# Kernel tuning notes

Hardware: AMD Instinct MI355X
Metric: run time of the kernel (lower is better)

The kernel has to match this reference:

```python
import jax, jax.numpy as jnp
import numpy as np

EPS = 1e-5

def _bn_relu(y, mean, var, scale, bias):
    # y: (b, c, n); eval-mode batchnorm over channel axis, then ReLU
    inv = scale / jnp.sqrt(var + EPS)
    return jax.nn.relu((y - mean[None, :, None]) * inv[None, :, None] + bias[None, :, None])

def setup_inputs() -> dict:
    key = jax.random.key(0)
    ks = jax.random.split(key, 6)
    b, c, n, cr = 4, 256, 4096, 32
    inp = {
        'x': jax.random.normal(ks[0], (b, c, n), jnp.float32),
        'w_q': jax.random.normal(ks[1], (cr, c), jnp.float32) * (1.0 / np.sqrt(c)),
        'w_k': jax.random.normal(ks[2], (cr, c), jnp.float32) * (1.0 / np.sqrt(c)),
        'w_v': jax.random.normal(ks[3], (c, c), jnp.float32) * (1.0 / np.sqrt(c)),
        'bn1_scale': jnp.ones((cr,), jnp.float32), 'bn1_bias': jnp.zeros((cr,), jnp.float32),
        'bn1_mean': jnp.zeros((cr,), jnp.float32), 'bn1_var': jnp.ones((cr,), jnp.float32),
        'bn2_scale': jnp.ones((cr,), jnp.float32), 'bn2_bias': jnp.zeros((cr,), jnp.float32),
        'bn2_mean': jnp.zeros((cr,), jnp.float32), 'bn2_var': jnp.ones((cr,), jnp.float32),
        'bn3_scale': jnp.ones((c,), jnp.float32), 'bn3_bias': jnp.zeros((c,), jnp.float32),
        'bn3_mean': jnp.zeros((c,), jnp.float32), 'bn3_var': jnp.ones((c,), jnp.float32),
        'gamma': jax.random.normal(ks[4], (1,), jnp.float32),
    }
    return inp

def reference(x, w_q, w_k, w_v,
              bn1_scale, bn1_bias, bn1_mean, bn1_var,
              bn2_scale, bn2_bias, bn2_mean, bn2_var,
              bn3_scale, bn3_bias, bn3_mean, bn3_var,
              gamma):
    # x: (b, c, n). Original views as (b, c, n, 1) so width=1, height=n.
    b, c, n = x.shape
    # 1x1 conv == channel matmul, then BN+ReLU
    q = _bn_relu(jnp.einsum('oc,bcn->bon', w_q, x), bn1_mean, bn1_var, bn1_scale, bn1_bias)  # (b, c', n)
    k = _bn_relu(jnp.einsum('oc,bcn->bon', w_k, x), bn2_mean, bn2_var, bn2_scale, bn2_bias)  # (b, c', n)
    v = _bn_relu(jnp.einsum('oc,bcn->bon', w_v, x), bn3_mean, bn3_var, bn3_scale, bn3_bias)  # (b, c, n)
    # energy_H: (b, n, n) with -inf diagonal (self-attention along 'height')
    energy_h = jnp.einsum('bdi,bdj->bij', q, k)
    eye = jnp.eye(n, dtype=bool)
    energy_h = jnp.where(eye[None], -jnp.inf, energy_h)
    # energy_W: width=1 -> per-position self energy (b, n)
    energy_w = jnp.sum(q * k, axis=1)
    # softmax over concat of n H-logits and 1 W-logit
    att = jax.nn.softmax(jnp.concatenate([energy_h, energy_w[..., None]], axis=-1), axis=-1)  # (b, n, n+1)
    att_h = att[..., :n]        # (b, n, n), query i -> key j
    att_w = att[..., n]         # (b, n)
    out_h = jnp.einsum('bcj,bij->bci', v, att_h)   # aggregate values along height
    out_w = v * att_w[:, None, :]                  # width=1 self term
    out = gamma[0] * (out_h + out_w) + x
    return out
```

## Files before the change

### kernel.cpp

```cpp
#include <hip/hip_runtime.h>
#include <math.h>

#define Bb 4
#define Cc 256
#define Nn 4096
#define CR 32
#define EPS_BN 1e-5f
#define SHIFT 20.0f
#define JSPLIT 4
#define JSL (Nn / JSPLIT)
#define TJ 64
#define NTILES (JSL / TJ)

typedef __attribute__((ext_vector_type(8))) short short8;
typedef __attribute__((ext_vector_type(4))) float f32x4;

__device__ inline unsigned int pk2(float a, float b) {
    __bf16 ha = (__bf16)a, hb = (__bf16)b;
    unsigned short ra = __builtin_bit_cast(unsigned short, ha);
    unsigned short rb = __builtin_bit_cast(unsigned short, hb);
    return ((unsigned int)rb << 16) | ra;
}
__device__ inline float blo(unsigned int u) { return __uint_as_float(u << 16); }
__device__ inline float bhi(unsigned int u) { return __uint_as_float(u & 0xffff0000u); }

__global__ __launch_bounds__(256) void xt_kernel(
    const float* __restrict__ x, __bf16* __restrict__ xTh, __bf16* __restrict__ xTl)
{
    __shared__ float sT[64][68];
    const int tid = threadIdx.x;
    const int n0 = blockIdx.x * 64, c0 = blockIdx.y * 64, b = blockIdx.z;
    const int n4 = tid & 15, cr = tid >> 4;
#pragma unroll
    for (int it = 0; it < 4; ++it) {
        int cl = cr + it * 16;
        float4 t = *(const float4*)&x[(size_t)(b * Cc + c0 + cl) * Nn + n0 + n4 * 4];
        *(float4*)&sT[cl][n4 * 4] = t;
    }
    __syncthreads();
    const int nl = tid >> 2, cq = tid & 3;
    float hv[16], lv[16];
#pragma unroll
    for (int e = 0; e < 16; ++e) {
        float v = sT[cq * 16 + e][nl];
        float h = (float)(__bf16)v;
        hv[e] = h; lv[e] = v - h;
    }
    uint4 H0 = { pk2(hv[0],hv[1]), pk2(hv[2],hv[3]), pk2(hv[4],hv[5]), pk2(hv[6],hv[7]) };
    uint4 H1 = { pk2(hv[8],hv[9]), pk2(hv[10],hv[11]), pk2(hv[12],hv[13]), pk2(hv[14],hv[15]) };
    uint4 L0 = { pk2(lv[0],lv[1]), pk2(lv[2],lv[3]), pk2(lv[4],lv[5]), pk2(lv[6],lv[7]) };
    uint4 L1 = { pk2(lv[8],lv[9]), pk2(lv[10],lv[11]), pk2(lv[12],lv[13]), pk2(lv[14],lv[15]) };
    size_t row = (size_t)(b * Nn + n0 + nl) * Cc + c0 + cq * 16;
    *(uint4*)&xTh[row] = H0; *(uint4*)&xTh[row + 8] = H1;
    *(uint4*)&xTl[row] = L0; *(uint4*)&xTl[row + 8] = L1;
}

__global__ __launch_bounds__(256) void qkv_kernel(
    const __bf16* __restrict__ xTh, const __bf16* __restrict__ xTl,
    const float* __restrict__ wq, const float* __restrict__ wk, const float* __restrict__ wv,
    const float* __restrict__ bn1s, const float* __restrict__ bn1b, const float* __restrict__ bn1m, const float* __restrict__ bn1v,
    const float* __restrict__ bn2s, const float* __restrict__ bn2b, const float* __restrict__ bn2m, const float* __restrict__ bn2v,
    const float* __restrict__ bn3s, const float* __restrict__ bn3b, const float* __restrict__ bn3m, const float* __restrict__ bn3v,
    __bf16* __restrict__ Qt, __bf16* __restrict__ Kt, __bf16* __restrict__ Vb)
{
    __shared__ __align__(16) __bf16 sW[64 * 264];

    const int tid = threadIdx.x;
    const int n0 = blockIdx.x * 128, g = blockIdx.y, b = blockIdx.z;
    const int lane = tid & 63, w = tid >> 6;
    const int l15 = lane & 15, l4 = lane >> 4;

    {
        int r = tid >> 2, q = tid & 3;
        int R = g * 64 + r;
        const float* src = (R < 32) ? (wq + (size_t)R * Cc)
                         : (R < 64) ? (wk + (size_t)(R - 32) * Cc)
                                    : (wv + (size_t)(R - 64) * Cc);
#pragma unroll
        for (int u8 = 0; u8 < 8; ++u8) {
            float4 a = *(const float4*)&src[q * 64 + u8 * 8];
            float4 c2 = *(const float4*)&src[q * 64 + u8 * 8 + 4];
            uint4 p = { pk2(a.x,a.y), pk2(a.z,a.w), pk2(c2.x,c2.y), pk2(c2.z,c2.w) };
            *(uint4*)&sW[r * 264 + q * 64 + u8 * 8] = p;
        }
    }
    __syncthreads();

    short8 af[8];
#pragma unroll
    for (int kc = 0; kc < 8; ++kc)
        af[kc] = *(const short8*)&sW[(w * 16 + l15) * 264 + kc * 32 + l4 * 8];

    f32x4 acc[8];
#pragma unroll
    for (int z = 0; z < 8; ++z) acc[z] = (f32x4){0.f, 0.f, 0.f, 0.f};

#pragma unroll
    for (int kc = 0; kc < 8; ++kc) {
#pragma unroll
        for (int nt = 0; nt < 8; ++nt) {
            size_t base = (size_t)(b * Nn + n0 + nt * 16 + l15) * Cc + kc * 32 + l4 * 8;
            short8 bh = *(const short8*)&xTh[base];
            short8 bl = *(const short8*)&xTl[base];
            acc[nt] = __builtin_amdgcn_mfma_f32_16x16x32_bf16(af[kc], bh, acc[nt], 0, 0, 0);
            acc[nt] = __builtin_amdgcn_mfma_f32_16x16x32_bf16(af[kc], bl, acc[nt], 0, 0, 0);
        }
    }

    float scl[4], off[4];
#pragma unroll
    for (int r = 0; r < 4; ++r) {
        int R = g * 64 + w * 16 + l4 * 4 + r;
        const float *bs, *bbi, *bm, *bv2; int row;
        if (R < 32)      { row = R;      bs = bn1s; bbi = bn1b; bm = bn1m; bv2 = bn1v; }
        else if (R < 64) { row = R - 32; bs = bn2s; bbi = bn2b; bm = bn2m; bv2 = bn2v; }
        else             { row = R - 64; bs = bn3s; bbi = bn3b; bm = bn3m; bv2 = bn3v; }
        float s = bs[row] / sqrtf(bv2[row] + EPS_BN);
        scl[r] = s; off[r] = bbi[row] - bm[row] * s;
    }

    if (g == 0) {
        __bf16* dst = (w < 2) ? Qt : Kt;
        int d0 = (w & 1) * 16 + l4 * 4;
#pragma unroll
        for (int nt = 0; nt < 8; ++nt) {
            f32x4 a = acc[nt];
            float e0 = fmaxf(fmaf(a.x, scl[0], off[0]), 0.f);
            float e1 = fmaxf(fmaf(a.y, scl[1], off[1]), 0.f);
            float e2 = fmaxf(fmaf(a.z, scl[2], off[2]), 0.f);
            float e3 = fmaxf(fmaf(a.w, scl[3], off[3]), 0.f);
            uint2 p = { pk2(e0, e1), pk2(e2, e3) };
            int n = n0 + nt * 16 + l15;
            *(uint2*)&dst[(size_t)(b * Nn + n) * CR + d0] = p;
        }
    } else {
        __bf16* oT = sW;
        __syncthreads();
#pragma unroll
        for (int nt = 0; nt < 8; ++nt) {
            f32x4 a = acc[nt];
            float e[4];
            e[0] = fmaxf(fmaf(a.x, scl[0], off[0]), 0.f);
            e[1] = fmaxf(fmaf(a.y, scl[1], off[1]), 0.f);
            e[2] = fmaxf(fmaf(a.z, scl[2], off[2]), 0.f);
            e[3] = fmaxf(fmaf(a.w, scl[3], off[3]), 0.f);
#pragma unroll
            for (int r = 0; r < 4; ++r)
                oT[(w * 16 + l4 * 4 + r) * 136 + nt * 16 + l15] = (__bf16)e[r];
        }
        __syncthreads();
        int rr = tid >> 2, qq = tid & 3;
        size_t vrow = (size_t)(b * Cc + (g - 1) * 64 + rr) * Nn + n0 + qq * 32;
#pragma unroll
        for (int e8 = 0; e8 < 4; ++e8)
            *(uint4*)&Vb[vrow + e8 * 8] = *(const uint4*)&oT[rr * 136 + qq * 32 + e8 * 8];
    }
}

__global__ __launch_bounds__(256) void attn_kernel(
    const __bf16* __restrict__ Qt, const __bf16* __restrict__ Kt,
    const __bf16* __restrict__ Vb,
    __bf16* __restrict__ PO, float* __restrict__ PL)
{
    __shared__ __align__(16) __bf16 sQ[64 * 40];
    __shared__ __align__(16) __bf16 sP[64 * 72];
    __shared__ __align__(16) float  sL[4][64];

    const int tid = threadIdx.x, lane = tid & 63, w = tid >> 6;
    const int b = blockIdx.z, js = blockIdx.y, i0 = blockIdx.x * 64;
    const int l15 = lane & 15, l4 = lane >> 4;

    {
        int i = tid >> 2, o = tid & 3;
        *(uint4*)&sQ[i * 40 + o * 8] =
            *(const uint4*)&Qt[(size_t)(b * Nn + i0 + i) * CR + o * 8];
    }
    __syncthreads();
    short8 qf[4];
#pragma unroll
    for (int it = 0; it < 4; ++it)
        qf[it] = *(const short8*)&sQ[(it * 16 + l15) * 40 + l4 * 8];

    f32x4 oacc[16];
#pragma unroll
    for (int z = 0; z < 16; ++z) oacc[z] = (f32x4){0.f, 0.f, 0.f, 0.f};
    float lp[4] = {0.f, 0.f, 0.f, 0.f};

    const size_t jb = (size_t)js * JSL;
    short8 kf = *(const short8*)&Kt[(size_t)(b * Nn + jb + 16 * w + l15) * CR + l4 * 8];

    for (int t = 0; t < NTILES; ++t) {
        const size_t j0 = jb + (size_t)t * TJ;

        short8 vf[8];
#pragma unroll
        for (int u = 0; u < 8; ++u) {
            int jh = u >> 2, ct = u & 3;
            int c = w * 64 + ct * 16 + l15;
            vf[u] = *(const short8*)&Vb[(size_t)(b * Cc + c) * Nn + j0 + (jh * 4 + l4) * 8];
        }

#pragma unroll
        for (int it = 0; it < 4; ++it) {
            f32x4 c0 = (f32x4){0.f, 0.f, 0.f, 0.f};
            c0 = __builtin_amdgcn_mfma_f32_16x16x32_bf16(kf, qf[it], c0, 0, 0, 0);
            float e0 = __expf(c0.x - SHIFT);
            float e1 = __expf(c0.y - SHIFT);
            float e2 = __expf(c0.z - SHIFT);
            float e3 = __expf(c0.w - SHIFT);
            lp[it] += (e0 + e1) + (e2 + e3);
            uint2 p2 = { pk2(e0, e1), pk2(e2, e3) };
            *(uint2*)&sP[(it * 16 + l15) * 72 + w * 16 + l4 * 4] = p2;
        }
        __syncthreads();

        if (t + 1 < NTILES)
            kf = *(const short8*)&Kt[(size_t)(b * Nn + j0 + TJ + 16 * w + l15) * CR + l4 * 8];

#pragma unroll
        for (int jh = 0; jh < 2; ++jh) {
            short8 pf[4];
#pragma unroll
            for (int it = 0; it < 4; ++it)
                pf[it] = *(const short8*)&sP[(it * 16 + l15) * 72 + jh * 32 + l4 * 8];
#pragma unroll
            for (int ct = 0; ct < 4; ++ct) {
#pragma unroll
                for (int it = 0; it < 4; ++it)
                    oacc[it * 4 + ct] = __builtin_amdgcn_mfma_f32_16x16x32_bf16(
                        pf[it], vf[jh * 4 + ct], oacc[it * 4 + ct], 0, 0, 0);
            }
        }
        __syncthreads();
    }

#pragma unroll
    for (int it = 0; it < 4; ++it) {
        float v = lp[it];
        v += __shfl_xor(v, 16);
        v += __shfl_xor(v, 32);
        if (lane < 16) sL[w][it * 16 + lane] = v;
    }
    __syncthreads();
    if (tid < 64)
        PL[(size_t)(js * Bb + b) * Nn + i0 + tid] =
            sL[0][tid] + sL[1][tid] + sL[2][tid] + sL[3][tid];

    const size_t base = (size_t)((js * Bb + b) * (Nn / 64) + blockIdx.x) * 16384;
#pragma unroll
    for (int it = 0; it < 4; ++it)
#pragma unroll
        for (int ct = 0; ct < 4; ++ct) {
            f32x4 a = oacc[it * 4 + ct];
            uint2 p = { pk2(a.x, a.y), pk2(a.z, a.w) };
            *(uint2*)&PO[base + (size_t)((((w * 4 + it) * 4 + ct) * 64 + lane)) * 4] = p;
        }
}

__global__ __launch_bounds__(256) void reduce_kernel(
    const __bf16* __restrict__ PO, const float* __restrict__ PL,
    const float* __restrict__ x, const float* __restrict__ gamma,
    float* __restrict__ out)
{
    __shared__ __align__(16) float oT[64 * 68];
    __shared__ float sLinv[64];

    const int tid = threadIdx.x;
    const int iblk = blockIdx.x, wq = blockIdx.y, b = blockIdx.z;
    const int i0 = iblk * 64;
    const int lane = tid & 63, ct = tid >> 6, l15 = lane & 15, l4 = lane >> 4;

    if (tid < 64) {
        float l = 0.f;
#pragma unroll
        for (int js = 0; js < JSPLIT; ++js)
            l += PL[(size_t)(js * Bb + b) * Nn + i0 + tid];
        sLinv[tid] = 1.0f / l;
    }

    float o[4][4];
#pragma unroll
    for (int it = 0; it < 4; ++it) {
        o[it][0] = o[it][1] = o[it][2] = o[it][3] = 0.f;
#pragma unroll
        for (int js = 0; js < JSPLIT; ++js) {
            size_t base = (size_t)((js * Bb + b) * (Nn / 64) + iblk) * 16384;
            uint2 v = *(const uint2*)&PO[base + (size_t)((((wq * 4 + it) * 4 + ct) * 64 + lane)) * 4];
            o[it][0] += blo(v.x); o[it][1] += bhi(v.x);
            o[it][2] += blo(v.y); o[it][3] += bhi(v.y);
        }
    }

    const int cl = ct * 16 + l15;
#pragma unroll
    for (int it = 0; it < 4; ++it) {
        float4 t4 = { o[it][0], o[it][1], o[it][2], o[it][3] };
        *(float4*)&oT[cl * 68 + it * 16 + l4 * 4] = t4;
    }
    __syncthreads();

    const float g = gamma[0];
    const int c_l = tid >> 2, icol = (tid & 3) * 16;
    const int cg = wq * 64 + c_l;
    const size_t gb = (size_t)(b * Cc + cg) * Nn + i0 + icol;
#pragma unroll
    for (int k4 = 0; k4 < 4; ++k4) {
        float4 ov = *(const float4*)&oT[c_l * 68 + icol + k4 * 4];
        float4 li = *(const float4*)&sLinv[icol + k4 * 4];
        float4 xv = *(const float4*)&x[gb + k4 * 4];
        float4 res;
        res.x = fmaf(g, ov.x * li.x, xv.x);
        res.y = fmaf(g, ov.y * li.y, xv.y);
        res.z = fmaf(g, ov.z * li.z, xv.z);
        res.w = fmaf(g, ov.w * li.w, xv.w);
        *(float4*)&out[gb + k4 * 4] = res;
    }
}

extern "C" void kernel_launch(void* const* d_in, const int* in_sizes, int n_in,
                              void* d_out, int out_size, void* d_ws, size_t ws_size,
                              hipStream_t stream)
{
    const float* x    = (const float*)d_in[0];
    const float* wq   = (const float*)d_in[1];
    const float* wk   = (const float*)d_in[2];
    const float* wv   = (const float*)d_in[3];
    const float* bn1s = (const float*)d_in[4];
    const float* bn1b = (const float*)d_in[5];
    const float* bn1m = (const float*)d_in[6];
    const float* bn1v = (const float*)d_in[7];
    const float* bn2s = (const float*)d_in[8];
    const float* bn2b = (const float*)d_in[9];
    const float* bn2m = (const float*)d_in[10];
    const float* bn2v = (const float*)d_in[11];
    const float* bn3s = (const float*)d_in[12];
    const float* bn3b = (const float*)d_in[13];
    const float* bn3m = (const float*)d_in[14];
    const float* bn3v = (const float*)d_in[15];
    const float* gmm  = (const float*)d_in[16];
    float* out = (float*)d_out;

    char* ws = (char*)d_ws;
    __bf16* Qt  = (__bf16*)(ws);
    __bf16* Kt  = (__bf16*)(ws + (1u << 20));
    __bf16* Vb  = (__bf16*)(ws + (2u << 20));
    char*   big = ws + (10u << 20);
    __bf16* xTh = (__bf16*)big;
    __bf16* xTl = (__bf16*)(big + 8388608);
    __bf16* PO  = (__bf16*)big;
    float*  PL  = (float*)(big + 33554432);

    xt_kernel<<<dim3(Nn / 64, Cc / 64, Bb), 256, 0, stream>>>(x, xTh, xTl);

    qkv_kernel<<<dim3(Nn / 128, 5, Bb), 256, 0, stream>>>(
        xTh, xTl, wq, wk, wv,
        bn1s, bn1b, bn1m, bn1v,
        bn2s, bn2b, bn2m, bn2v,
        bn3s, bn3b, bn3m, bn3v,
        Qt, Kt, Vb);

    attn_kernel<<<dim3(Nn / 64, JSPLIT, Bb), 256, 0, stream>>>(Qt, Kt, Vb, PO, PL);

    reduce_kernel<<<dim3(Nn / 64, 4, Bb), 256, 0, stream>>>(PO, PL, x, gmm, out);
}
```

Baseline: 235.9 us.

## Remap attention blocks per XCD, stage x tiles in LDS, use exp2 softmax

The attention grid is flattened and remapped so that blocks sharing a (j-split, batch) pair land on the same XCD, which should improve L2 reuse of K and V. The QKV kernel now stages x hi/lo tiles through shared memory with register prefetch instead of reading them directly from global memory, at the cost of two barriers per k-chunk. K is prescaled by log2(e) so the softmax can use native exp2 with an adjusted shift. The transpose kernel rotates its LDS read order to reduce bank conflicts, and the BN scale uses rsqrt instead of a division.

```diff
diff --git a/kernel.cpp b/kernel.cpp
--- a/kernel.cpp
+++ b/kernel.cpp
@@ -1,12 +1,12 @@
 #include <hip/hip_runtime.h>
-#include <math.h>
 
 #define Bb 4
 #define Cc 256
 #define Nn 4096
 #define CR 32
 #define EPS_BN 1e-5f
-#define SHIFT 20.0f
+#define SHIFT2 28.853900817779268f
+#define LOG2E  1.4426950408889634f
 #define JSPLIT 4
 #define JSL (Nn / JSPLIT)
 #define TJ 64
@@ -23,6 +23,7 @@
 }
 __device__ inline float blo(unsigned int u) { return __uint_as_float(u << 16); }
 __device__ inline float bhi(unsigned int u) { return __uint_as_float(u & 0xffff0000u); }
+__device__ inline float ex2(float x) { return __builtin_amdgcn_exp2f(x); }
 
 __global__ __launch_bounds__(256) void xt_kernel(
     const float* __restrict__ x, __bf16* __restrict__ xTh, __bf16* __restrict__ xTl)
@@ -41,7 +42,8 @@
     const int nl = tid >> 2, cq = tid & 3;
     float hv[16], lv[16];
 #pragma unroll
-    for (int e = 0; e < 16; ++e) {
+    for (int ee = 0; ee < 16; ++ee) {
+        int e = (ee + 4 * cq) & 15;
         float v = sT[cq * 16 + e][nl];
         float h = (float)(__bf16)v;
         hv[e] = h; lv[e] = v - h;
@@ -63,7 +65,10 @@
     const float* __restrict__ bn3s, const float* __restrict__ bn3b, const float* __restrict__ bn3m, const float* __restrict__ bn3v,
     __bf16* __restrict__ Qt, __bf16* __restrict__ Kt, __bf16* __restrict__ Vb)
 {
-    __shared__ __align__(16) __bf16 sW[64 * 264];
+    __shared__ __align__(16) char uL[64 * 264 * 2];
+    __bf16* sW = (__bf16*)uL;
+    __bf16* sX = (__bf16*)uL;
+    __bf16* oT = (__bf16*)uL;
 
     const int tid = threadIdx.x;
     const int n0 = blockIdx.x * 128, g = blockIdx.y, b = blockIdx.z;
@@ -85,23 +90,37 @@
         }
     }
     __syncthreads();
-
     short8 af[8];
 #pragma unroll
     for (int kc = 0; kc < 8; ++kc)
         af[kc] = *(const short8*)&sW[(w * 16 + l15) * 264 + kc * 32 + l4 * 8];
 
+    const int xp = tid >> 7;
+    const int xn = tid & 127;
+    const __bf16* xsrc = (xp ? xTl : xTh) + (size_t)(b * Nn + n0 + xn) * Cc;
+    uint4 xbuf[4];
+#pragma unroll
+    for (int s = 0; s < 4; ++s) xbuf[s] = *(const uint4*)&xsrc[s * 8];
+
     f32x4 acc[8];
 #pragma unroll
     for (int z = 0; z < 8; ++z) acc[z] = (f32x4){0.f, 0.f, 0.f, 0.f};
 
-#pragma unroll
     for (int kc = 0; kc < 8; ++kc) {
+        __syncthreads();
+#pragma unroll
+        for (int s = 0; s < 4; ++s)
+            *(uint4*)&sX[(xp * 128 + xn) * 40 + s * 8] = xbuf[s];
+        __syncthreads();
+        if (kc + 1 < 8) {
+#pragma unroll
+            for (int s = 0; s < 4; ++s)
+                xbuf[s] = *(const uint4*)&xsrc[(kc + 1) * 32 + s * 8];
+        }
 #pragma unroll
         for (int nt = 0; nt < 8; ++nt) {
-            size_t base = (size_t)(b * Nn + n0 + nt * 16 + l15) * Cc + kc * 32 + l4 * 8;
-            short8 bh = *(const short8*)&xTh[base];
-            short8 bl = *(const short8*)&xTl[base];
+            short8 bh = *(const short8*)&sX[(nt * 16 + l15) * 40 + l4 * 8];
+            short8 bl = *(const short8*)&sX[(128 + nt * 16 + l15) * 40 + l4 * 8];
             acc[nt] = __builtin_amdgcn_mfma_f32_16x16x32_bf16(af[kc], bh, acc[nt], 0, 0, 0);
             acc[nt] = __builtin_amdgcn_mfma_f32_16x16x32_bf16(af[kc], bl, acc[nt], 0, 0, 0);
         }
@@ -115,8 +134,10 @@
         if (R < 32)      { row = R;      bs = bn1s; bbi = bn1b; bm = bn1m; bv2 = bn1v; }
         else if (R < 64) { row = R - 32; bs = bn2s; bbi = bn2b; bm = bn2m; bv2 = bn2v; }
         else             { row = R - 64; bs = bn3s; bbi = bn3b; bm = bn3m; bv2 = bn3v; }
-        float s = bs[row] / sqrtf(bv2[row] + EPS_BN);
-        scl[r] = s; off[r] = bbi[row] - bm[row] * s;
+        float s = bs[row] * __frsqrt_rn(bv2[row] + EPS_BN);
+        float o = bbi[row] - bm[row] * s;
+        if (g == 0 && R >= 32) { s *= LOG2E; o *= LOG2E; }
+        scl[r] = s; off[r] = o;
     }
 
     if (g == 0) {
@@ -134,7 +155,6 @@
             *(uint2*)&dst[(size_t)(b * Nn + n) * CR + d0] = p;
         }
     } else {
-        __bf16* oT = sW;
         __syncthreads();
 #pragma unroll
         for (int nt = 0; nt < 8; ++nt) {
@@ -167,7 +187,12 @@
     __shared__ __align__(16) float  sL[4][64];
 
     const int tid = threadIdx.x, lane = tid & 63, w = tid >> 6;
-    const int b = blockIdx.z, js = blockIdx.y, i0 = blockIdx.x * 64;
+    const int id = blockIdx.x;
+    const int xcd = id & 7, k = id >> 3;
+    const int js = xcd >> 1;
+    const int b  = (xcd & 1) * 2 + (k & 1);
+    const int iblk = k >> 1;
+    const int i0 = iblk * 64;
     const int l15 = lane & 15, l4 = lane >> 4;
 
     {
@@ -204,10 +229,10 @@
         for (int it = 0; it < 4; ++it) {
             f32x4 c0 = (f32x4){0.f, 0.f, 0.f, 0.f};
             c0 = __builtin_amdgcn_mfma_f32_16x16x32_bf16(kf, qf[it], c0, 0, 0, 0);
-            float e0 = __expf(c0.x - SHIFT);
-            float e1 = __expf(c0.y - SHIFT);
-            float e2 = __expf(c0.z - SHIFT);
-            float e3 = __expf(c0.w - SHIFT);
+            float e0 = ex2(c0.x - SHIFT2);
+            float e1 = ex2(c0.y - SHIFT2);
+            float e2 = ex2(c0.z - SHIFT2);
+            float e3 = ex2(c0.w - SHIFT2);
             lp[it] += (e0 + e1) + (e2 + e3);
             uint2 p2 = { pk2(e0, e1), pk2(e2, e3) };
             *(uint2*)&sP[(it * 16 + l15) * 72 + w * 16 + l4 * 4] = p2;
@@ -246,7 +271,7 @@
         PL[(size_t)(js * Bb + b) * Nn + i0 + tid] =
             sL[0][tid] + sL[1][tid] + sL[2][tid] + sL[3][tid];
 
-    const size_t base = (size_t)((js * Bb + b) * (Nn / 64) + blockIdx.x) * 16384;
+    const size_t base = (size_t)((js * Bb + b) * (Nn / 64) + iblk) * 16384;
 #pragma unroll
     for (int it = 0; it < 4; ++it)
 #pragma unroll
@@ -359,7 +384,7 @@
         bn3s, bn3b, bn3m, bn3v,
         Qt, Kt, Vb);
 
-    attn_kernel<<<dim3(Nn / 64, JSPLIT, Bb), 256, 0, stream>>>(Qt, Kt, Vb, PO, PL);
+    attn_kernel<<<dim3(JSPLIT * Bb * (Nn / 64)), 256, 0, stream>>>(Qt, Kt, Vb, PO, PL);
 
     reduce_kernel<<<dim3(Nn / 64, 4, Bb), 256, 0, stream>>>(PO, PL, x, gmm, out);
 }
```

Result: slower. 277.4 us (+17.6%).
